# Kernel optimization log

Measured on AMD Instinct MI355X. Metric: run time of the kernel, lower is better.

Reference implementation:

```python
import jax, jax.numpy as jnp
import numpy as np

N_NODES = 25000
N_EDGES = 400000
EMBED_DIM = 128
NUM_HEADS = 8
D_K = EMBED_DIM // NUM_HEADS


def setup_inputs() -> dict:
    key = jax.random.key(0)
    ks = jax.random.split(key, 8)
    sc = 1.0 / np.sqrt(EMBED_DIM)
    return {
        "x": jax.random.normal(ks[0], (N_NODES, EMBED_DIM), jnp.float32),
        "edge_index": jax.random.randint(ks[1], (2, N_EDGES), 0, N_NODES),
        "attn_bias": jax.random.normal(ks[2], (N_EDGES, NUM_HEADS), jnp.float32),
        "Wq": jax.random.normal(ks[3], (EMBED_DIM, EMBED_DIM), jnp.float32) * sc,
        "bq": jnp.zeros((EMBED_DIM,), jnp.float32),
        "Wk": jax.random.normal(ks[4], (EMBED_DIM, EMBED_DIM), jnp.float32) * sc,
        "bk": jnp.zeros((EMBED_DIM,), jnp.float32),
        "Wv": jax.random.normal(ks[5], (EMBED_DIM, EMBED_DIM), jnp.float32) * sc,
        "bv": jnp.zeros((EMBED_DIM,), jnp.float32),
        "Wo": jax.random.normal(ks[6], (EMBED_DIM, EMBED_DIM), jnp.float32) * sc,
        "bo": jnp.zeros((EMBED_DIM,), jnp.float32),
    }


def reference(x, edge_index, attn_bias, Wq, bq, Wk, bk, Wv, bv, Wo, bo):
    N = x.shape[0]
    E = edge_index.shape[1]
    H, dk = NUM_HEADS, D_K
    scale = 1.0 / np.sqrt(dk).astype(np.float32)
    dst = edge_index[0]  # query/aggregation node per edge
    src = edge_index[1]  # key/value node per edge

    # project at node level (as torch: linear(x)[index]), then gather per edge
    q = (x @ Wq.T + bq)[dst].reshape(E, H, dk)
    k = (x @ Wk.T + bk)[src].reshape(E, H, dk)
    v = (x @ Wv.T + bv)[src].reshape(E, H, dk)

    logits = scale * jnp.sum(q * k, axis=2) + attn_bias  # [E, H]

    # segment softmax over edges grouped by destination node
    m = jax.ops.segment_max(logits, dst, num_segments=N)     # [N, H]
    e = jnp.exp(logits - m[dst])                              # [E, H]
    z = jax.ops.segment_sum(e, dst, num_segments=N)           # [N, H]
    scores = e / z[dst]                                       # [E, H]

    agg = jax.ops.segment_sum(scores[..., None] * v, dst, num_segments=N)  # [N, H, dk]
    out = agg.reshape(N, H * dk) @ Wo.T + bo                   # [N, embed_dim]
    return out, logits[..., None]
```

## Files before the change

kernel.cpp:

```cpp
#include <hip/hip_runtime.h>
#include <math.h>

#define N_NODES 25000
#define N_EDGES 400000
#define EMBED   128
#define HEADS   8
#define DK      16
#define MAXDEG  96
#define NX (N_NODES * 128)

typedef __attribute__((ext_vector_type(8))) short bf16x8;
typedef __attribute__((ext_vector_type(4))) float f32x4;
typedef unsigned int uint;
typedef unsigned short ushort;

__device__ inline uint pack2_bf16(float a, float b) {
    union { float f; uint u; } ua, ub;
    ua.f = a; ub.f = b;
    uint ra = (ua.u + 0x7FFFu + ((ua.u >> 16) & 1u)) >> 16;
    uint rb = (ub.u + 0x7FFFu + ((ub.u >> 16) & 1u)) >> 16;
    return (ra & 0xFFFFu) | (rb << 16);
}
__device__ inline ushort cvt_bf16(float a) {
    union { float f; uint u; } ua; ua.f = a;
    return (ushort)((ua.u + 0x7FFFu + ((ua.u >> 16) & 1u)) >> 16);
}
__device__ inline float bf16_lo(uint u) {
    union { uint u; float f; } x; x.u = u << 16; return x.f;
}
__device__ inline float bf16_hi(uint u) {
    union { uint u; float f; } x; x.u = u & 0xFFFF0000u; return x.f;
}

__global__ __launch_bounds__(256) void prep(
    const float* __restrict__ Wq, const float* __restrict__ Wk,
    const float* __restrict__ Wv, const float* __restrict__ Wo,
    ushort* __restrict__ wb, int* __restrict__ deg)
{
    int i = blockIdx.x * 256 + threadIdx.x;
    if (i < N_NODES) deg[i] = 0;
    if (i < 32768) {
        int j = i * 2;
        const float* src = (j < 16384) ? Wq + j
                         : (j < 32768) ? Wk + (j - 16384)
                         : (j < 49152) ? Wv + (j - 32768)
                         :               Wo + (j - 49152);
        float2 v = *reinterpret_cast<const float2*>(src);
        reinterpret_cast<uint*>(wb)[i] = pack2_bf16(v.x, v.y);
    }
}

__global__ __launch_bounds__(256) void scatter_edges(
    const int* __restrict__ ei, int* __restrict__ deg,
    int2* __restrict__ csr2)
{
    int e = blockIdx.x * 256 + threadIdx.x;
    if (e >= N_EDGES) return;
    int dst = ei[e];
    int src = ei[N_EDGES + e];
    int pos = atomicAdd(&deg[dst], 1);
    if (pos < MAXDEG) csr2[dst * MAXDEG + pos] = make_int2(e, src);
}

__global__ __launch_bounds__(256) void gemm_qkv(
    const float* __restrict__ x, const ushort* __restrict__ Wall,
    const float* __restrict__ bq, const float* __restrict__ bk,
    const float* __restrict__ bv,
    ushort* __restrict__ Qb, ushort* __restrict__ Kb, ushort* __restrict__ Vb)
{
    const int lane = threadIdx.x & 63;
    const int wave = threadIdx.x >> 6;
    const int ml   = lane & 15;
    const int quad = lane >> 4;
    const int m0   = blockIdx.x * 64 + wave * 16;

    int arow = m0 + ml; if (arow >= N_NODES) arow = N_NODES - 1;
    const float* xp = x + arow * 128 + quad * 8;

    bf16x8 af[4];
#pragma unroll
    for (int ks = 0; ks < 4; ++ks) {
        float4 a0 = *reinterpret_cast<const float4*>(xp + ks * 32);
        float4 a1 = *reinterpret_cast<const float4*>(xp + ks * 32 + 4);
        uint* u = reinterpret_cast<uint*>(&af[ks]);
        u[0] = pack2_bf16(a0.x, a0.y); u[1] = pack2_bf16(a0.z, a0.w);
        u[2] = pack2_bf16(a1.x, a1.y); u[3] = pack2_bf16(a1.z, a1.w);
    }

#pragma unroll
    for (int which = 0; which < 3; ++which) {
        const ushort* W = Wall + which * 16384;
        f32x4 acc[8];
#pragma unroll
        for (int ct = 0; ct < 8; ++ct) acc[ct] = (f32x4){0.f, 0.f, 0.f, 0.f};

#pragma unroll
        for (int ks = 0; ks < 4; ++ks) {
#pragma unroll
            for (int ct = 0; ct < 8; ++ct) {
                bf16x8 bf = *reinterpret_cast<const bf16x8*>(
                    W + (ct * 16 + ml) * 128 + ks * 32 + quad * 8);
                acc[ct] = __builtin_amdgcn_mfma_f32_16x16x32_bf16(af[ks], bf, acc[ct], 0, 0, 0);
            }
        }

        const float* bias = (which == 0) ? bq : (which == 1) ? bk : bv;
        ushort* C = (which == 0) ? Qb : (which == 1) ? Kb : Vb;
#pragma unroll
        for (int ct = 0; ct < 8; ++ct) {
            int col = ct * 16 + ml;
            float b = bias[col];
#pragma unroll
            for (int r = 0; r < 4; ++r) {
                int row = m0 + quad * 4 + r;
                if (row < N_NODES)
                    C[row * 128 + col] = cvt_bf16(acc[ct][r] + b);
            }
        }
    }
}

__global__ __launch_bounds__(256) void gemm_out(
    const ushort* __restrict__ A, const ushort* __restrict__ W,
    const float* __restrict__ bias, float* __restrict__ C, int M)
{
    const int lane = threadIdx.x & 63;
    const int wave = threadIdx.x >> 6;
    const int ml   = lane & 15;
    const int quad = lane >> 4;
    const int m0   = blockIdx.x * 64 + wave * 16;

    int arow = m0 + ml; if (arow >= M) arow = M - 1;
    const ushort* ap = A + arow * 128 + quad * 8;

    f32x4 acc[8];
#pragma unroll
    for (int ct = 0; ct < 8; ++ct) acc[ct] = (f32x4){0.f, 0.f, 0.f, 0.f};

#pragma unroll
    for (int ks = 0; ks < 128; ks += 32) {
        bf16x8 af = *reinterpret_cast<const bf16x8*>(ap + ks);
#pragma unroll
        for (int ct = 0; ct < 8; ++ct) {
            bf16x8 bf = *reinterpret_cast<const bf16x8*>(
                W + (ct * 16 + ml) * 128 + ks + quad * 8);
            acc[ct] = __builtin_amdgcn_mfma_f32_16x16x32_bf16(af, bf, acc[ct], 0, 0, 0);
        }
    }

#pragma unroll
    for (int ct = 0; ct < 8; ++ct) {
        int col = ct * 16 + ml;
        float bv_ = bias[col];
#pragma unroll
        for (int r = 0; r < 4; ++r) {
            int row = m0 + quad * 4 + r;
            if (row < M)
                C[row * 128 + col] = acc[ct][r] + bv_;
        }
    }
}

__global__ __launch_bounds__(256) void fused_attn(
    const ushort* __restrict__ Q2, const ushort* __restrict__ K2,
    const ushort* __restrict__ V2,
    const float* __restrict__ attn_bias,
    const int* __restrict__ deg, const int2* __restrict__ csr2,
    float* __restrict__ logits, ushort* __restrict__ AGG)
{
    const int lane = threadIdx.x & 63;
    const int wid  = threadIdx.x >> 6;
    const int n = blockIdx.x * 4 + wid;
    int dg = deg[n]; if (dg > MAXDEG) dg = MAXDEG;
    const int start = n * MAXDEG;
    const int h  = lane & 7;
    const int es = lane >> 3;

    const uint4* Qu4 = reinterpret_cast<const uint4*>(Q2);
    const uint4* Ku4 = reinterpret_cast<const uint4*>(K2);
    const uint4* Vu4 = reinterpret_cast<const uint4*>(V2);

    uint4 qa = Qu4[n * 16 + h * 2];
    uint4 qb = Qu4[n * 16 + h * 2 + 1];
    float qf[16];
    {
        uint qq[8] = {qa.x, qa.y, qa.z, qa.w, qb.x, qb.y, qb.z, qb.w};
#pragma unroll
        for (int j = 0; j < 8; ++j) {
            qf[2 * j]     = bf16_lo(qq[j]);
            qf[2 * j + 1] = bf16_hi(qq[j]);
        }
    }

    float acc[16];
#pragma unroll
    for (int j = 0; j < 16; ++j) acc[j] = 0.f;
    float z = 0.f;

    if (dg > 0) {
        int2 ep = csr2[start + (es < dg ? es : dg - 1)];
        for (int base = 0; base < dg; base += 8) {
            int e = ep.x, s = ep.y;
            bool valid = (base + es) < dg;

            uint4 k0 = Ku4[s * 16 + h * 2];
            uint4 k1 = Ku4[s * 16 + h * 2 + 1];
            uint4 v0 = Vu4[s * 16 + h * 2];
            uint4 v1 = Vu4[s * 16 + h * 2 + 1];
            float bias = attn_bias[e * 8 + h];

            int nb = base + 8;
            if (nb < dg) {
                int t2 = nb + es; if (t2 >= dg) t2 = dg - 1;
                ep = csr2[start + t2];
            }

            uint kk[8] = {k0.x, k0.y, k0.z, k0.w, k1.x, k1.y, k1.z, k1.w};
            float d = 0.f;
#pragma unroll
            for (int j = 0; j < 8; ++j)
                d += qf[2 * j] * bf16_lo(kk[j]) + qf[2 * j + 1] * bf16_hi(kk[j]);

            float l = 0.25f * d + bias;
            float p = 0.f;
            if (valid) {
                __builtin_nontemporal_store(l, &logits[e * 8 + h]);
                p = __expf(l);
            }
            z += p;

            uint vv[8] = {v0.x, v0.y, v0.z, v0.w, v1.x, v1.y, v1.z, v1.w};
#pragma unroll
            for (int j = 0; j < 8; ++j) {
                acc[2 * j]     += p * bf16_lo(vv[j]);
                acc[2 * j + 1] += p * bf16_hi(vv[j]);
            }
        }
    }

    {
        int bit = (lane >> 5) & 1;
#pragma unroll
        for (int j = 0; j < 8; ++j) {
            float send = bit ? acc[j] : acc[j + 8];
            float keep = bit ? acc[j + 8] : acc[j];
            acc[j] = keep + __shfl_xor(send, 32, 64);
        }
        bit = (lane >> 4) & 1;
#pragma unroll
        for (int j = 0; j < 4; ++j) {
            float send = bit ? acc[j] : acc[j + 4];
            float keep = bit ? acc[j + 4] : acc[j];
            acc[j] = keep + __shfl_xor(send, 16, 64);
        }
        bit = (lane >> 3) & 1;
#pragma unroll
        for (int j = 0; j < 2; ++j) {
            float send = bit ? acc[j] : acc[j + 2];
            float keep = bit ? acc[j + 2] : acc[j];
            acc[j] = keep + __shfl_xor(send, 8, 64);
        }
    }
    z += __shfl_xor(z, 8, 64);
    z += __shfl_xor(z, 16, 64);
    z += __shfl_xor(z, 32, 64);

    float inv = (z > 0.f) ? 1.f / z : 0.f;
    int d_off = ((lane >> 5) & 1) * 8 + ((lane >> 4) & 1) * 4 + ((lane >> 3) & 1) * 2;
    reinterpret_cast<uint*>(AGG)[n * 64 + h * 8 + (d_off >> 1)] =
        pack2_bf16(acc[0] * inv, acc[1] * inv);
}

extern "C" void kernel_launch(void* const* d_in, const int* in_sizes, int n_in,
                              void* d_out, int out_size, void* d_ws, size_t ws_size,
                              hipStream_t stream)
{
    const float* x         = (const float*)d_in[0];
    const int*   ei        = (const int*)  d_in[1];
    const float* attn_bias = (const float*)d_in[2];
    const float* Wq = (const float*)d_in[3];
    const float* bq = (const float*)d_in[4];
    const float* Wk = (const float*)d_in[5];
    const float* bk = (const float*)d_in[6];
    const float* Wv = (const float*)d_in[7];
    const float* bv = (const float*)d_in[8];
    const float* Wo = (const float*)d_in[9];
    const float* bo = (const float*)d_in[10];

    float* out    = (float*)d_out;
    float* logits = out + N_NODES * EMBED;

    ushort* wb   = (ushort*)d_ws;
    ushort* Qb   = wb + 4 * 16384;
    ushort* Kb   = Qb + NX;
    ushort* Vb   = Kb + NX;
    ushort* AGGb = Vb + NX;
    int* deg     = (int*)(AGGb + NX);
    int2* csr2   = (int2*)(deg + N_NODES);

    prep<<<128, 256, 0, stream>>>(Wq, Wk, Wv, Wo, wb, deg);

    scatter_edges<<<(N_EDGES + 255) / 256, 256, 0, stream>>>(ei, deg, csr2);

    int gblocks = (N_NODES + 63) / 64;
    gemm_qkv<<<gblocks, 256, 0, stream>>>(x, wb, bq, bk, bv, Qb, Kb, Vb);

    fused_attn<<<N_NODES / 4, 256, 0, stream>>>(Qb, Kb, Vb, attn_bias,
                                                deg, csr2, logits, AGGb);

    gemm_out<<<gblocks, 256, 0, stream>>>(AGGb, wb + 3 * 16384, bo, out, N_NODES);
}
```

Measured before the change: 203.0 us.

## Merge prep with edge scatter and split GEMMs across more blocks

Measured after the change: 198.5 us. 1.02x faster.

```diff
diff --git a/kernel.cpp b/kernel.cpp
--- a/kernel.cpp
+++ b/kernel.cpp
@@ -8,6 +8,7 @@
 #define DK      16
 #define MAXDEG  96
 #define NX (N_NODES * 128)
+#define SCAT_BLOCKS ((N_EDGES + 255) / 256)
 
 typedef __attribute__((ext_vector_type(8))) short bf16x8;
 typedef __attribute__((ext_vector_type(4))) float f32x4;
@@ -32,14 +33,15 @@
     union { uint u; float f; } x; x.u = u & 0xFFFF0000u; return x.f;
 }
 
-__global__ __launch_bounds__(256) void prep(
+__global__ __launch_bounds__(256) void prep_scatter(
     const float* __restrict__ Wq, const float* __restrict__ Wk,
     const float* __restrict__ Wv, const float* __restrict__ Wo,
-    ushort* __restrict__ wb, int* __restrict__ deg)
-{
-    int i = blockIdx.x * 256 + threadIdx.x;
-    if (i < N_NODES) deg[i] = 0;
-    if (i < 32768) {
+    ushort* __restrict__ wb,
+    const int* __restrict__ ei, int* __restrict__ deg,
+    int2* __restrict__ csr2)
+{
+    if (blockIdx.x < 128) {
+        int i = blockIdx.x * 256 + threadIdx.x;
         int j = i * 2;
         const float* src = (j < 16384) ? Wq + j
                          : (j < 32768) ? Wk + (j - 16384)
@@ -47,19 +49,14 @@
                          :               Wo + (j - 49152);
         float2 v = *reinterpret_cast<const float2*>(src);
         reinterpret_cast<uint*>(wb)[i] = pack2_bf16(v.x, v.y);
-    }
-}
-
-__global__ __launch_bounds__(256) void scatter_edges(
-    const int* __restrict__ ei, int* __restrict__ deg,
-    int2* __restrict__ csr2)
-{
-    int e = blockIdx.x * 256 + threadIdx.x;
-    if (e >= N_EDGES) return;
-    int dst = ei[e];
-    int src = ei[N_EDGES + e];
-    int pos = atomicAdd(&deg[dst], 1);
-    if (pos < MAXDEG) csr2[dst * MAXDEG + pos] = make_int2(e, src);
+    } else {
+        int e = (blockIdx.x - 128) * 256 + threadIdx.x;
+        if (e >= N_EDGES) return;
+        int dst = ei[e];
+        int src = ei[N_EDGES + e];
+        int pos = atomicAdd(&deg[dst], 1);
+        if (pos < MAXDEG) csr2[dst * MAXDEG + pos] = make_int2(e, src);
+    }
 }
 
 __global__ __launch_bounds__(256) void gemm_qkv(
@@ -68,6 +65,11 @@
     const float* __restrict__ bv,
     ushort* __restrict__ Qb, ushort* __restrict__ Kb, ushort* __restrict__ Vb)
 {
+    const int which = blockIdx.y;
+    const ushort* W = Wall + which * 16384;
+    const float* bias = (which == 0) ? bq : (which == 1) ? bk : bv;
+    ushort* C = (which == 0) ? Qb : (which == 1) ? Kb : Vb;
+
     const int lane = threadIdx.x & 63;
     const int wave = threadIdx.x >> 6;
     const int ml   = lane & 15;
@@ -87,35 +89,29 @@
         u[2] = pack2_bf16(a1.x, a1.y); u[3] = pack2_bf16(a1.z, a1.w);
     }
 
-#pragma unroll
-    for (int which = 0; which < 3; ++which) {
-        const ushort* W = Wall + which * 16384;
-        f32x4 acc[8];
-#pragma unroll
-        for (int ct = 0; ct < 8; ++ct) acc[ct] = (f32x4){0.f, 0.f, 0.f, 0.f};
-
-#pragma unroll
-        for (int ks = 0; ks < 4; ++ks) {
-#pragma unroll
-            for (int ct = 0; ct < 8; ++ct) {
-                bf16x8 bf = *reinterpret_cast<const bf16x8*>(
-                    W + (ct * 16 + ml) * 128 + ks * 32 + quad * 8);
-                acc[ct] = __builtin_amdgcn_mfma_f32_16x16x32_bf16(af[ks], bf, acc[ct], 0, 0, 0);
-            }
-        }
-
-        const float* bias = (which == 0) ? bq : (which == 1) ? bk : bv;
-        ushort* C = (which == 0) ? Qb : (which == 1) ? Kb : Vb;
+    f32x4 acc[8];
+#pragma unroll
+    for (int ct = 0; ct < 8; ++ct) acc[ct] = (f32x4){0.f, 0.f, 0.f, 0.f};
+
+#pragma unroll
+    for (int ks = 0; ks < 4; ++ks) {
 #pragma unroll
         for (int ct = 0; ct < 8; ++ct) {
-            int col = ct * 16 + ml;
-            float b = bias[col];
-#pragma unroll
-            for (int r = 0; r < 4; ++r) {
-                int row = m0 + quad * 4 + r;
-                if (row < N_NODES)
-                    C[row * 128 + col] = cvt_bf16(acc[ct][r] + b);
-            }
+            bf16x8 bf = *reinterpret_cast<const bf16x8*>(
+                W + (ct * 16 + ml) * 128 + ks * 32 + quad * 8);
+            acc[ct] = __builtin_amdgcn_mfma_f32_16x16x32_bf16(af[ks], bf, acc[ct], 0, 0, 0);
+        }
+    }
+
+#pragma unroll
+    for (int ct = 0; ct < 8; ++ct) {
+        int col = ct * 16 + ml;
+        float b = bias[col];
+#pragma unroll
+        for (int r = 0; r < 4; ++r) {
+            int row = m0 + quad * 4 + r;
+            if (row < N_NODES)
+                C[row * 128 + col] = cvt_bf16(acc[ct][r] + b);
         }
     }
 }
@@ -129,28 +125,29 @@
     const int ml   = lane & 15;
     const int quad = lane >> 4;
     const int m0   = blockIdx.x * 64 + wave * 16;
+    const int ct0  = blockIdx.y * 4;
 
     int arow = m0 + ml; if (arow >= M) arow = M - 1;
     const ushort* ap = A + arow * 128 + quad * 8;
 
-    f32x4 acc[8];
-#pragma unroll
-    for (int ct = 0; ct < 8; ++ct) acc[ct] = (f32x4){0.f, 0.f, 0.f, 0.f};
+    f32x4 acc[4];
+#pragma unroll
+    for (int ct = 0; ct < 4; ++ct) acc[ct] = (f32x4){0.f, 0.f, 0.f, 0.f};
 
 #pragma unroll
     for (int ks = 0; ks < 128; ks += 32) {
         bf16x8 af = *reinterpret_cast<const bf16x8*>(ap + ks);
 #pragma unroll
-        for (int ct = 0; ct < 8; ++ct) {
+        for (int ct = 0; ct < 4; ++ct) {
             bf16x8 bf = *reinterpret_cast<const bf16x8*>(
-                W + (ct * 16 + ml) * 128 + ks + quad * 8);
+                W + ((ct0 + ct) * 16 + ml) * 128 + ks + quad * 8);
             acc[ct] = __builtin_amdgcn_mfma_f32_16x16x32_bf16(af, bf, acc[ct], 0, 0, 0);
         }
     }
 
 #pragma unroll
-    for (int ct = 0; ct < 8; ++ct) {
-        int col = ct * 16 + ml;
+    for (int ct = 0; ct < 4; ++ct) {
+        int col = (ct0 + ct) * 16 + ml;
         float bv_ = bias[col];
 #pragma unroll
         for (int r = 0; r < 4; ++r) {
@@ -298,15 +295,17 @@
     int* deg     = (int*)(AGGb + NX);
     int2* csr2   = (int2*)(deg + N_NODES);
 
-    prep<<<128, 256, 0, stream>>>(Wq, Wk, Wv, Wo, wb, deg);
-
-    scatter_edges<<<(N_EDGES + 255) / 256, 256, 0, stream>>>(ei, deg, csr2);
+    hipMemsetAsync(deg, 0, N_NODES * sizeof(int), stream);
+
+    prep_scatter<<<128 + SCAT_BLOCKS, 256, 0, stream>>>(Wq, Wk, Wv, Wo, wb,
+                                                        ei, deg, csr2);
 
     int gblocks = (N_NODES + 63) / 64;
-    gemm_qkv<<<gblocks, 256, 0, stream>>>(x, wb, bq, bk, bv, Qb, Kb, Vb);
+    gemm_qkv<<<dim3(gblocks, 3), 256, 0, stream>>>(x, wb, bq, bk, bv, Qb, Kb, Vb);
 
     fused_attn<<<N_NODES / 4, 256, 0, stream>>>(Qb, Kb, Vb, attn_bias,
                                                 deg, csr2, logits, AGGb);
 
-    gemm_out<<<gblocks, 256, 0, stream>>>(AGGb, wb + 3 * 16384, bo, out, N_NODES);
-}
+    gemm_out<<<dim3(gblocks, 2), 256, 0, stream>>>(AGGb, wb + 3 * 16384, bo,
+                                                   out, N_NODES);
+}
```
